# Kernel tuning notes

Measured on AMD Instinct MI355X. Metric: run time of the kernel, lower is better.

Reference implementation:

```python
import jax, jax.numpy as jnp
import numpy as np

RAD2DEG = 180.0 / 3.14159  # module uses 3.14159, not pi

def _conv2d(x, w):
    # x: (N,1,H,W), w: (O,1,3,3), SAME padding, stride 1
    return jax.lax.conv_general_dilated(
        x, w, window_strides=(1, 1), padding='SAME',
        dimension_numbers=('NCHW', 'OIHW', 'NCHW'))

def _make_filters():
    sobel = np.array([[1, 0, -1], [2, 0, -2], [1, 0, -1]], dtype=np.float32)
    f0   = [[0,0,0],[0,1,-1],[0,0,0]]
    f45  = [[0,0,0],[0,1,0],[0,0,-1]]
    f90  = [[0,0,0],[0,1,0],[0,-1,0]]
    f135 = [[0,0,0],[0,1,0],[-1,0,0]]
    f180 = [[0,0,0],[-1,1,0],[0,0,0]]
    f225 = [[-1,0,0],[0,1,0],[0,0,0]]
    f270 = [[0,-1,0],[0,1,0],[0,0,0]]
    f315 = [[0,0,-1],[0,1,0],[0,0,0]]
    dirs = np.stack([f0,f45,f90,f135,f180,f225,f270,f315]).astype(np.float32)
    return sobel, dirs

def setup_inputs() -> dict:
    key = jax.random.key(0)
    H, W = 2160, 3840
    img = jax.random.uniform(key, (1, 3, H, W), dtype=jnp.float32)
    sobel, dirs = _make_filters()
    sobel_h = jnp.asarray(sobel)[None, None]          # (1,1,3,3)
    sobel_v = jnp.asarray(sobel.T)[None, None]        # (1,1,3,3)
    dir_w = jnp.asarray(dirs)[:, None]                # (8,1,3,3)
    return {"img": img, "sobel_h": sobel_h, "sobel_v": sobel_v, "dir_w": dir_w}

def reference(img, sobel_h, sobel_v, dir_w):
    # grayscale: mean of the 3 channels
    gray = (img[:, 0:1] + img[:, 1:2] + img[:, 2:3]) / 3.0        # (1,1,H,W)
    grad_x = _conv2d(gray, sobel_h)
    grad_y = _conv2d(gray, sobel_v)
    grad_mag = jnp.sqrt(grad_x ** 2 + grad_y ** 2)                # (1,1,H,W)
    # orientation in degrees, snapped to multiples of 45 (round-half-even, like torch.round)
    ori = jnp.round((jnp.arctan2(grad_y, grad_x) * RAD2DEG + 180.0) / 45.0)
    idx_pos = jnp.mod(ori, 8.0).astype(jnp.int32)                 # (1,1,H,W)
    idx_neg = jnp.mod(ori + 4.0, 8.0).astype(jnp.int32)
    all_filtered = _conv2d(grad_mag, dir_w)                       # (1,8,H,W)
    # per-pixel channel select (the flattened gather in the original)
    pos = jnp.take_along_axis(all_filtered, idx_pos, axis=1)      # (1,1,H,W)
    neg = jnp.take_along_axis(all_filtered, idx_neg, axis=1)
    is_max = jnp.minimum(pos, neg) > 0.0
    # in-place aliasing in the original: thin_edges/early_threshold alias grad_mag,
    # so the final binary map is: is_max AND (grad_mag >= 0.2)
    th = jnp.where(is_max & (grad_mag >= 0.2), 1.0, 0.0).astype(jnp.float32)
    return th
```

## Files before the change

kernel.cpp:

```cpp
#include <hip/hip_runtime.h>
#include <math.h>

#define IMG_W 3840
#define IMG_H 2160
#define TW 124
#define TH 16
#define LW 128
#define GROWS (TH + 4)
#define MROWS (TH + 2)

#define DXPACK 0x901A
#define DYPACK 0x1A9

#define T1_SLOPE 0.41421317376456f
#define T2_SLOPE 2.41420676743300f
#define SECT_EPS 3.0e-5f

__device__ __noinline__ int slow_sector(float sx, float sy) {
#pragma clang fp contract(off)
    const float RADF = (float)(180.0 / 3.14159);
    float t = atan2f(sy, sx);
    float wv = ((t * RADF) + 180.0f) / 45.0f;
    float ori = rintf(wv);
    float fr = fabsf(wv - ori);
    if (fr > 0.4995f) {
        double td = atan2((double)sy, (double)sx);
        float t2 = (float)td;
        wv = ((t2 * RADF) + 180.0f) / 45.0f;
        ori = rintf(wv);
    }
    return ((int)ori) & 7;
}

__global__ __launch_bounds__(256) void canny_like_kernel(const float* __restrict__ img,
                                                         float* __restrict__ out) {
#pragma clang fp contract(off)
    __shared__ float lds_g[GROWS][LW];
    __shared__ float lds_m[MROWS][LW];
    __shared__ short lds_o[MROWS][LW];

    const int c = threadIdx.x;
    const int h = threadIdx.y;
    const int gx = blockIdx.x * TW - 2 + c;
    const int gy0 = blockIdx.y * TH - 2;
    const bool xok = (unsigned)gx < (unsigned)IMG_W;

    const float* p = img + gx;
    for (int i = 0; i < GROWS / 2; ++i) {
        int gy = gy0 + 2 * i + h;
        float v = 0.0f;
        if (xok && (unsigned)gy < (unsigned)IMG_H) {
            long o = (long)gy * IMG_W;
            float c0 = p[o];
            float c1 = p[o + (long)IMG_W * IMG_H];
            float c2 = p[o + 2l * IMG_W * IMG_H];
            v = ((c0 + c1) + c2) / 3.0f;
        }
        lds_g[2 * i + h][c] = v;
    }
    __syncthreads();

    if (c >= 1 && c <= 126) {
        for (int i = 0; i < MROWS / 2; ++i) {
            int r = 2 * i + h;
            int gy = gy0 + 1 + r;
            float mag = 0.0f;
            short offp = 0;
            if (xok && (unsigned)gy < (unsigned)IMG_H) {
                float a00 = lds_g[r][c - 1],     a01 = lds_g[r][c],     a02 = lds_g[r][c + 1];
                float a10 = lds_g[r + 1][c - 1],                        a12 = lds_g[r + 1][c + 1];
                float a20 = lds_g[r + 2][c - 1], a21 = lds_g[r + 2][c], a22 = lds_g[r + 2][c + 1];
                float sx = a00;
                sx = sx - a02;
                sx = sx + 2.0f * a10;
                sx = sx - 2.0f * a12;
                sx = sx + a20;
                sx = sx - a22;
                float sy = a00;
                sy = sy + 2.0f * a01;
                sy = sy + a02;
                sy = sy - a20;
                sy = sy - 2.0f * a21;
                sy = sy - a22;
                mag = sqrtf(sx * sx + sy * sy);

                float ax = fabsf(sx), ay = fabsf(sy);
                float d1 = fmaf(-T1_SLOPE, ax, ay);
                float d2 = fmaf(-T2_SLOPE, ax, ay);
                float s = ax + ay;
                int dxo, dyo;
                if (fabsf(d1) < SECT_EPS * s || fabsf(d2) < SECT_EPS * s) {
                    int idx = slow_sector(sx, sy);
                    dxo = ((DXPACK >> (2 * idx)) & 3) - 1;
                    dyo = ((DYPACK >> (2 * idx)) & 3) - 1;
                } else {
                    dxo = (d2 > 0.0f) ? 0 : ((sx > 0.0f) ? -1 : 1);
                    dyo = (d1 < 0.0f) ? 0 : ((sy > 0.0f) ? -1 : 1);
                }
                offp = (short)(dyo * LW + dxo);
            }
            lds_m[r][c] = mag;
            lds_o[r][c] = offp;
        }
    }
    __syncthreads();

    if (c >= 2 && c <= 125 && xok) {
        for (int i = 0; i < TH / 2; ++i) {
            int oy = 2 * i + h;
            int mr = oy + 1;
            float mc = lds_m[mr][c];
            int off = lds_o[mr][c];
            const float* mb = &lds_m[mr][c];
            float mp = mb[off];
            float mn = mb[-off];
            float res = (fminf(mc - mp, mc - mn) > 0.0f && mc >= 0.2f) ? 1.0f : 0.0f;
            out[(long)(gy0 + 2 + oy) * IMG_W + gx] = res;
        }
    }
}

extern "C" void kernel_launch(void* const* d_in, const int* in_sizes, int n_in,
                              void* d_out, int out_size, void* d_ws, size_t ws_size,
                              hipStream_t stream) {
    const float* img = (const float*)d_in[0];
    float* out = (float*)d_out;
    dim3 grid((IMG_W + TW - 1) / TW, IMG_H / TH);
    dim3 block(LW, 2);
    canny_like_kernel<<<grid, block, 0, stream>>>(img, out);
}
```

Baseline: 172.6 us.

## Stream rows per wavefront with shuffle-based Sobel and wave-local LDS suppression

Each 64-lane wavefront now owns a 60-pixel-wide column strip and walks down 20 output rows. It keeps a rolling three-row window of grayscale values in registers and uses lane shuffles for the horizontal neighbours, so the grayscale LDS tile is gone. Magnitudes go to a per-wave LDS ring, and non-maximum suppression for the previous row is done in the same iteration. This removes the block-wide __syncthreads barriers and the staged LDS passes. The cost is a per-wave sequential dependency chain over rows, more register pressure from the full unroll, and two halo lanes wasted on each side of every wave.

```diff
diff --git a/kernel.cpp b/kernel.cpp
--- a/kernel.cpp
+++ b/kernel.cpp
@@ -3,11 +3,10 @@
 
 #define IMG_W 3840
 #define IMG_H 2160
-#define TW 124
-#define TH 16
-#define LW 128
-#define GROWS (TH + 4)
-#define MROWS (TH + 2)
+#define OUTW  60
+#define R     20
+#define ITERS (R + 4)
+#define MROWS (R + 2)
 
 #define DXPACK 0x901A
 #define DYPACK 0x1A9
@@ -32,90 +31,91 @@
     return ((int)ori) & 7;
 }
 
-__global__ __launch_bounds__(256) void canny_like_kernel(const float* __restrict__ img,
-                                                         float* __restrict__ out) {
+__global__ __launch_bounds__(256, 4) void canny_like_kernel(const float* __restrict__ img,
+                                                            float* __restrict__ out) {
 #pragma clang fp contract(off)
-    __shared__ float lds_g[GROWS][LW];
-    __shared__ float lds_m[MROWS][LW];
-    __shared__ short lds_o[MROWS][LW];
+    __shared__ float lds_m[4][MROWS][64];
 
-    const int c = threadIdx.x;
-    const int h = threadIdx.y;
-    const int gx = blockIdx.x * TW - 2 + c;
-    const int gy0 = blockIdx.y * TH - 2;
-    const bool xok = (unsigned)gx < (unsigned)IMG_W;
+    const int lane = threadIdx.x;
+    const int w    = threadIdx.y;
+    const int X0   = (blockIdx.x * 4 + w) * OUTW;
+    const int Y0   = blockIdx.y * R;
+    const int x    = X0 - 2 + lane;
+    const bool xok    = (unsigned)x < (unsigned)IMG_W;
+    const int  xc     = min(max(x, 0), IMG_W - 1);
+    const bool xmok   = (lane >= 1) && (lane <= 62) && xok;
+    const bool xoutok = (lane >= 2) && (lane <= 61);
 
-    const float* p = img + gx;
-    for (int i = 0; i < GROWS / 2; ++i) {
-        int gy = gy0 + 2 * i + h;
-        float v = 0.0f;
-        if (xok && (unsigned)gy < (unsigned)IMG_H) {
-            long o = (long)gy * IMG_W;
-            float c0 = p[o];
-            float c1 = p[o + (long)IMG_W * IMG_H];
-            float c2 = p[o + 2l * IMG_W * IMG_H];
-            v = ((c0 + c1) + c2) / 3.0f;
+    const float* im1 = img + (size_t)IMG_W * IMG_H;
+    const float* im2 = img + 2 * (size_t)IMG_W * IMG_H;
+
+    float gl[3], gc[3], gr[3];
+    float mc_p = 0.0f;
+    int   off_p = 0;
+
+#pragma unroll
+    for (int k = 0; k < ITERS; ++k) {
+        const int y = Y0 - 2 + k;
+        float g = 0.0f;
+        if ((unsigned)y < (unsigned)IMG_H) {
+            int o = y * IMG_W + xc;
+            float c0 = img[o], c1 = im1[o], c2 = im2[o];
+            float t = ((c0 + c1) + c2) / 3.0f;
+            g = xok ? t : 0.0f;
         }
-        lds_g[2 * i + h][c] = v;
-    }
-    __syncthreads();
+        const int s = k % 3;
+        gc[s] = g;
+        gl[s] = __shfl_up(g, 1);
+        gr[s] = __shfl_down(g, 1);
 
-    if (c >= 1 && c <= 126) {
-        for (int i = 0; i < MROWS / 2; ++i) {
-            int r = 2 * i + h;
-            int gy = gy0 + 1 + r;
-            float mag = 0.0f;
-            short offp = 0;
-            if (xok && (unsigned)gy < (unsigned)IMG_H) {
-                float a00 = lds_g[r][c - 1],     a01 = lds_g[r][c],     a02 = lds_g[r][c + 1];
-                float a10 = lds_g[r + 1][c - 1],                        a12 = lds_g[r + 1][c + 1];
-                float a20 = lds_g[r + 2][c - 1], a21 = lds_g[r + 2][c], a22 = lds_g[r + 2][c + 1];
-                float sx = a00;
-                sx = sx - a02;
-                sx = sx + 2.0f * a10;
-                sx = sx - 2.0f * a12;
-                sx = sx + a20;
-                sx = sx - a22;
-                float sy = a00;
-                sy = sy + 2.0f * a01;
-                sy = sy + a02;
-                sy = sy - a20;
-                sy = sy - 2.0f * a21;
-                sy = sy - a22;
-                mag = sqrtf(sx * sx + sy * sy);
+        if (k >= 2) {
+            const int i0 = (k - 2) % 3, i1 = (k - 1) % 3, i2 = k % 3;
+            float a00 = gl[i0], a01 = gc[i0], a02 = gr[i0];
+            float a10 = gl[i1],               a12 = gr[i1];
+            float a20 = gl[i2], a21 = gc[i2], a22 = gr[i2];
+            float sx = a00;
+            sx = sx - a02;
+            sx = sx + 2.0f * a10;
+            sx = sx - 2.0f * a12;
+            sx = sx + a20;
+            sx = sx - a22;
+            float sy = a00;
+            sy = sy + 2.0f * a01;
+            sy = sy + a02;
+            sy = sy - a20;
+            sy = sy - 2.0f * a21;
+            sy = sy - a22;
+            float magv = sqrtf(sx * sx + sy * sy);
 
-                float ax = fabsf(sx), ay = fabsf(sy);
-                float d1 = fmaf(-T1_SLOPE, ax, ay);
-                float d2 = fmaf(-T2_SLOPE, ax, ay);
-                float s = ax + ay;
-                int dxo, dyo;
-                if (fabsf(d1) < SECT_EPS * s || fabsf(d2) < SECT_EPS * s) {
-                    int idx = slow_sector(sx, sy);
-                    dxo = ((DXPACK >> (2 * idx)) & 3) - 1;
-                    dyo = ((DYPACK >> (2 * idx)) & 3) - 1;
-                } else {
-                    dxo = (d2 > 0.0f) ? 0 : ((sx > 0.0f) ? -1 : 1);
-                    dyo = (d1 < 0.0f) ? 0 : ((sy > 0.0f) ? -1 : 1);
-                }
-                offp = (short)(dyo * LW + dxo);
+            float ax = fabsf(sx), ay = fabsf(sy);
+            float d1 = fmaf(-T1_SLOPE, ax, ay);
+            float d2 = fmaf(-T2_SLOPE, ax, ay);
+            float sA = ax + ay;
+            int dxo, dyo;
+            if (__builtin_expect(fabsf(d1) < SECT_EPS * sA || fabsf(d2) < SECT_EPS * sA, 0)) {
+                int idx = slow_sector(sx, sy);
+                dxo = ((DXPACK >> (2 * idx)) & 3) - 1;
+                dyo = ((DYPACK >> (2 * idx)) & 3) - 1;
+            } else {
+                dxo = (d2 > 0.0f) ? 0 : ((sx > 0.0f) ? -1 : 1);
+                dyo = (d1 < 0.0f) ? 0 : ((sy > 0.0f) ? -1 : 1);
             }
-            lds_m[r][c] = mag;
-            lds_o[r][c] = offp;
-        }
-    }
-    __syncthreads();
+            const bool vok = xmok && ((unsigned)(y - 1) < (unsigned)IMG_H);
+            float mag = vok ? magv : 0.0f;
+            int  offv = vok ? (dyo * 64 + dxo) : 0;
 
-    if (c >= 2 && c <= 125 && xok) {
-        for (int i = 0; i < TH / 2; ++i) {
-            int oy = 2 * i + h;
-            int mr = oy + 1;
-            float mc = lds_m[mr][c];
-            int off = lds_o[mr][c];
-            const float* mb = &lds_m[mr][c];
-            float mp = mb[off];
-            float mn = mb[-off];
-            float res = (fminf(mc - mp, mc - mn) > 0.0f && mc >= 0.2f) ? 1.0f : 0.0f;
-            out[(long)(gy0 + 2 + oy) * IMG_W + gx] = res;
+            lds_m[w][k - 2][lane] = mag;
+
+            if (k >= 4) {
+                const float* cb = &lds_m[w][k - 3][lane];
+                float mp = cb[off_p];
+                float mn = cb[-off_p];
+                float res = (fminf(mc_p - mp, mc_p - mn) > 0.0f && mc_p >= 0.2f) ? 1.0f : 0.0f;
+                if (xoutok)
+                    out[(size_t)(Y0 + k - 4) * IMG_W + x] = res;
+            }
+            mc_p = mag;
+            off_p = offv;
         }
     }
 }
@@ -125,7 +125,7 @@
                               hipStream_t stream) {
     const float* img = (const float*)d_in[0];
     float* out = (float*)d_out;
-    dim3 grid((IMG_W + TW - 1) / TW, IMG_H / TH);
-    dim3 block(LW, 2);
+    dim3 grid(64 / 4, IMG_H / R);
+    dim3 block(64, 4);
     canny_like_kernel<<<grid, block, 0, stream>>>(img, out);
 }
```

New measurement: 166.3 us. 1.04x faster.
